# Performance work log

Hardware: AMD Instinct MI355X
Metric: run time of the kernel (lower is better)

The kernel has to match this reference:

```python
import jax, jax.numpy as jnp
import numpy as np

N_NODES = 50000
N_EDGES = 800000
F_IN = 128
HIDDEN = 128
F_OUT = 64
BN_EPS = 1e-5


def setup_inputs() -> dict:
    key = jax.random.key(0)
    ks = jax.random.split(key, 8)
    features = jax.random.normal(ks[0], (N_NODES, F_IN), dtype=jnp.float32)
    W1 = jax.random.normal(ks[1], (2 * F_IN, HIDDEN), dtype=jnp.float32) * 0.05
    b1 = jnp.zeros((HIDDEN,), dtype=jnp.float32)
    gamma = jnp.ones((HIDDEN,), dtype=jnp.float32)
    beta = jnp.zeros((HIDDEN,), dtype=jnp.float32)
    W2 = jax.random.normal(ks[2], (2 * HIDDEN, F_OUT), dtype=jnp.float32) * 0.05
    b2 = jnp.zeros((F_OUT,), dtype=jnp.float32)
    edge_vals = jax.random.uniform(ks[3], (N_EDGES,), dtype=jnp.float32)
    edge_src = jax.random.randint(ks[4], (N_EDGES,), 0, N_NODES, dtype=jnp.int32)
    edge_dst = jax.random.randint(ks[5], (N_EDGES,), 0, N_NODES, dtype=jnp.int32)
    return {"features": features, "W1": W1, "b1": b1, "gamma": gamma,
            "beta": beta, "W2": W2, "b2": b2, "edge_vals": edge_vals,
            "edge_src": edge_src, "edge_dst": edge_dst}


def _spmm(edge_vals, edge_src, edge_dst, x):
    # agg[i] = sum_{e: dst_e == i} w_e * x[src_e]   (sparse adjacency @ x)
    msgs = edge_vals[:, None] * x[edge_src]          # [E, d]
    return jax.ops.segment_sum(msgs, edge_dst, num_segments=N_NODES)


def _batchnorm(x, gamma, beta):
    # BatchNorm1d in training mode: batch stats, biased variance
    mean = jnp.mean(x, axis=0)
    var = jnp.mean(jnp.square(x - mean), axis=0)
    return gamma * (x - mean) * jax.lax.rsqrt(var + BN_EPS) + beta


def reference(features, W1, b1, gamma, beta, W2, b2, edge_vals, edge_src, edge_dst):
    # Layer 1: SpMM -> concat -> linear -> batchnorm -> relu  (dropout is a no-op, p=0)
    agg = _spmm(edge_vals, edge_src, edge_dst, features)     # [N, F_IN]
    s = jnp.concatenate([agg, features], axis=1)             # [N, 2*F_IN]
    h = s @ W1 + b1                                          # [N, HIDDEN]
    h = jax.nn.relu(_batchnorm(h, gamma, beta))
    # Layer 2: SpMM -> concat -> linear (identity act, no norm)
    agg2 = _spmm(edge_vals, edge_src, edge_dst, h)           # [N, HIDDEN]
    s2 = jnp.concatenate([agg2, h], axis=1)                  # [N, 2*HIDDEN]
    out = s2 @ W2 + b2                                       # [N, F_OUT]
    return out
```

## Files before the change

### kernel.cpp

```cpp
#include <hip/hip_runtime.h>

#define N_NODES 50000
#define N_EDGES 800000
#define F_IN    128
#define HID     128
#define F_OUT   64
#define BN_EPS  1e-5f

#define NRANGES 196
#define NCHUNKS 196
#define CHUNK   4096

typedef __bf16 bf16x8 __attribute__((ext_vector_type(8)));
typedef float  f32x4  __attribute__((ext_vector_type(4)));

static inline size_t align_up(size_t x, size_t a){ return (x + a - 1) / a * a; }

__device__ __forceinline__ float bflo(unsigned u){ return __uint_as_float(u << 16); }
__device__ __forceinline__ float bfhi(unsigned u){ return __uint_as_float(u & 0xffff0000u); }
__device__ __forceinline__ unsigned packbf(float a, float b){
  __bf16 ha = (__bf16)a, hb = (__bf16)b;
  unsigned short ua = __builtin_bit_cast(unsigned short, ha);
  unsigned short ub = __builtin_bit_cast(unsigned short, hb);
  return (unsigned)ua | ((unsigned)ub << 16);
}


__global__ __launch_bounds__(256) void k_pass1(const int* __restrict__ dst, int* __restrict__ Hcr){
  __shared__ int hist[NRANGES];
  int c = blockIdx.x, t = threadIdx.x;
  if(t < NRANGES) hist[t] = 0;
  __syncthreads();
  int e0 = c * CHUNK;
  #pragma unroll
  for(int k = 0; k < CHUNK / 256; k++){
    int e = e0 + k * 256 + t;
    if(e < N_EDGES) atomicAdd(&hist[dst[e] >> 8], 1);
  }
  __syncthreads();
  if(t < NRANGES) Hcr[c * NRANGES + t] = hist[t];
}

__global__ __launch_bounds__(256) void k_scanH(int* __restrict__ Hcr, int* __restrict__ rangeScan,
                                               float* __restrict__ bn_acc){
  __shared__ int s[256];
  int t = threadIdx.x;
  int run = 0;
  if(t < NRANGES){
    for(int c = 0; c < NCHUNKS; c++){
      int v = Hcr[c * NRANGES + t];
      Hcr[c * NRANGES + t] = run;
      run += v;
    }
  }
  s[t] = (t < NRANGES) ? run : 0;
  __syncthreads();
  for(int off = 1; off < 256; off <<= 1){
    int v = (t >= off) ? s[t - off] : 0;
    __syncthreads();
    s[t] += v;
    __syncthreads();
  }
  if(t < NRANGES) rangeScan[t + 1] = s[t];
  if(t == 0) rangeScan[0] = 0;
  bn_acc[t] = 0.f;
}

__global__ __launch_bounds__(256) void k_pass2(const int* __restrict__ dst, const int* __restrict__ src,
    const float* __restrict__ vals, const int* __restrict__ Hcr,
    const int* __restrict__ rangeScan, int2* __restrict__ staged){
  __shared__ int cur[NRANGES];
  int c = blockIdx.x, t = threadIdx.x;
  if(t < NRANGES) cur[t] = rangeScan[t] + Hcr[c * NRANGES + t];
  __syncthreads();
  int e0 = c * CHUNK;
  #pragma unroll
  for(int k = 0; k < CHUNK / 256; k++){
    int e = e0 + k * 256 + t;
    if(e < N_EDGES){
      int d = dst[e];
      int pos = atomicAdd(&cur[d >> 8], 1);
      staged[pos] = make_int2(__float_as_int(vals[e]), src[e] | ((d & 255) << 16));
    }
  }
}

__global__ __launch_bounds__(256) void k_pass3(const int2* __restrict__ staged,
    const int* __restrict__ rangeScan, int2* __restrict__ epack, int* __restrict__ rp){
  __shared__ int cnt[256];
  __shared__ int pre[256];
  int r = blockIdx.x, t = threadIdx.x;
  int beg = rangeScan[r], end = rangeScan[r + 1];
  cnt[t] = 0;
  __syncthreads();
  for(int i = beg + t; i < end; i += 256)
    atomicAdd(&cnt[(staged[i].y >> 16) & 255], 1);
  __syncthreads();
  int v = cnt[t];
  pre[t] = v;
  __syncthreads();
  for(int off = 1; off < 256; off <<= 1){
    int u = (t >= off) ? pre[t - off] : 0;
    __syncthreads();
    pre[t] += u;
    __syncthreads();
  }
  int excl = pre[t] - v;
  int d = r * 256 + t;
  if(d < N_NODES) rp[d] = beg + excl;
  if(r == NRANGES - 1 && t == 0) rp[N_NODES] = N_EDGES;
  __syncthreads();
  cnt[t] = beg + excl;
  __syncthreads();
  for(int i = beg + t; i < end; i += 256){
    int2 e = staged[i];
    int dl = (e.y >> 16) & 255;
    int p = atomicAdd(&cnt[dl], 1);
    epack[p] = make_int2(e.x, e.y & 0xffff);
  }
}


__global__ void k_prepW(const float* __restrict__ W1, const float* __restrict__ W2,
                        __bf16* __restrict__ W1f, __bf16* __restrict__ W2f){
  int t = blockIdx.x * 256 + threadIdx.x;
  if(t < 4096){
    int ks = t >> 9, rem = t & 511, nf = rem >> 6, l = rem & 63;
    int k = ks * 32 + (l >> 4) * 8, c = nf * 16 + (l & 15);
    bf16x8 v;
    #pragma unroll
    for(int i = 0; i < 8; i++) v[i] = (__bf16)W1[(size_t)(k + i) * HID + c];
    *(bf16x8*)(W1f + ((size_t)t << 3)) = v;
  } else if(t < 6144){
    int s = t - 4096;
    int ks = s >> 9, rem = s & 511, nf = rem >> 6, l = rem & 63;
    int k = ks * 32 + (l >> 4) * 8, c = nf * 16 + (l & 15);
    bf16x8 v;
    #pragma unroll
    for(int i = 0; i < 8; i++){
      int kk = k + i;
      float val = (c < 64) ? W2[(size_t)kk * F_OUT + c]
                           : W2[(size_t)(HID + kk) * F_OUT + (c - 64)];
      v[i] = (__bf16)val;
    }
    *(bf16x8*)(W2f + ((size_t)s << 3)) = v;
  }
}


__global__ __launch_bounds__(256) void k_cvtX(const float* __restrict__ X, __bf16* __restrict__ Sx){
  int t = blockIdx.x * 256 + threadIdx.x;
  if(t >= N_NODES * 16) return;
  int n = t >> 4;
  int c = (t & 15) * 8;
  const float* xp = X + (size_t)n * F_IN + c;
  f32x4 x0 = *(const f32x4*)xp;
  f32x4 x1 = *(const f32x4*)(xp + 4);
  bf16x8 v;
  #pragma unroll
  for(int i = 0; i < 4; i++){ v[i] = (__bf16)x0[i]; v[4 + i] = (__bf16)x1[i]; }
  *(bf16x8*)(Sx + (size_t)n * 128 + c) = v;
}


__global__ __launch_bounds__(256) void k_spmm1(const __bf16* __restrict__ Sx,
    __bf16* __restrict__ Sa, const int2* __restrict__ epack, const int* __restrict__ rp){
  int w    = (int)((blockIdx.x * blockDim.x + threadIdx.x) >> 6);
  int lane = threadIdx.x & 63;
  if(w >= N_NODES) return;
  int beg = rp[w], end = rp[w + 1];
  float a0 = 0.f, a1 = 0.f;
  int e = beg;
  for(; e + 3 < end; e += 4){
    int2 p0 = epack[e], p1 = epack[e + 1], p2 = epack[e + 2], p3 = epack[e + 3];
    unsigned u0 = *(const unsigned*)(Sx + (size_t)p0.y * 128 + lane * 2);
    unsigned u1 = *(const unsigned*)(Sx + (size_t)p1.y * 128 + lane * 2);
    unsigned u2 = *(const unsigned*)(Sx + (size_t)p2.y * 128 + lane * 2);
    unsigned u3 = *(const unsigned*)(Sx + (size_t)p3.y * 128 + lane * 2);
    float w0 = __int_as_float(p0.x), w1 = __int_as_float(p1.x);
    float w2 = __int_as_float(p2.x), w3 = __int_as_float(p3.x);
    a0 = fmaf(w0, bflo(u0), a0); a1 = fmaf(w0, bfhi(u0), a1);
    a0 = fmaf(w1, bflo(u1), a0); a1 = fmaf(w1, bfhi(u1), a1);
    a0 = fmaf(w2, bflo(u2), a0); a1 = fmaf(w2, bfhi(u2), a1);
    a0 = fmaf(w3, bflo(u3), a0); a1 = fmaf(w3, bfhi(u3), a1);
  }
  for(; e < end; e++){
    int2 p = epack[e];
    float wt = __int_as_float(p.x);
    unsigned u = *(const unsigned*)(Sx + (size_t)p.y * 128 + lane * 2);
    a0 = fmaf(wt, bflo(u), a0); a1 = fmaf(wt, bfhi(u), a1);
  }
  *(unsigned*)(Sa + (size_t)w * 128 + lane * 2) = packbf(a0, a1);
}


__global__ __launch_bounds__(256) void k_gemm1(
    const __bf16* __restrict__ Sa, const __bf16* __restrict__ Sx,
    const __bf16* __restrict__ W1f, const float* __restrict__ b1,
    __bf16* __restrict__ hpre, float* __restrict__ bn_acc){
  __shared__ float bnred[2][256];
  const int tid = threadIdx.x;
  const int lane = tid & 63, wid = tid >> 6;
  const int wm = wid >> 1, wn = wid & 1;
  const int lr = lane & 15, lk = (lane >> 4) * 8;
  const int rbase = blockIdx.x * 64 + wm * 32 + lr;

  f32x4 acc[2][4];
  #pragma unroll
  for(int m = 0; m < 2; m++)
    #pragma unroll
    for(int n = 0; n < 4; n++) acc[m][n] = (f32x4){0.f, 0.f, 0.f, 0.f};

  for(int ks = 0; ks < 8; ks++){
    const __bf16* src = (ks < 4) ? Sa : Sx;
    const int kb = (ks & 3) * 32 + lk;
    bf16x8 a[2], b[4];
    #pragma unroll
    for(int m = 0; m < 2; m++){
      int r = rbase + m * 16; if(r > N_NODES - 1) r = N_NODES - 1;
      a[m] = *(const bf16x8*)(src + (size_t)r * 128 + kb);
    }
    #pragma unroll
    for(int n = 0; n < 4; n++)
      b[n] = *(const bf16x8*)(W1f + (((ks * 8 + wn * 4 + n) * 64 + lane) << 3));
    #pragma unroll
    for(int m = 0; m < 2; m++)
      #pragma unroll
      for(int n = 0; n < 4; n++)
        acc[m][n] = __builtin_amdgcn_mfma_f32_16x16x32_bf16(a[m], b[n], acc[m][n], 0, 0, 0);
  }

  #pragma unroll
  for(int n = 0; n < 4; n++){
    int gc = wn * 64 + n * 16 + lr;
    float bias = b1[gc];
    float ps = 0.f, pq = 0.f;
    #pragma unroll
    for(int m = 0; m < 2; m++){
      int gr0 = blockIdx.x * 64 + wm * 32 + m * 16 + (lane >> 4) * 4;
      #pragma unroll
      for(int i = 0; i < 4; i++){
        int r = gr0 + i;
        if(r < N_NODES){
          float h = acc[m][n][i] + bias;
          hpre[(size_t)r * HID + gc] = (__bf16)h;
          ps += h; pq += h * h;
        }
      }
    }
    ps += __shfl_xor(ps, 16); ps += __shfl_xor(ps, 32);
    pq += __shfl_xor(pq, 16); pq += __shfl_xor(pq, 32);
    if(lane < 16){
      bnred[wm][gc] = ps;
      bnred[wm][128 + gc] = pq;
    }
  }
  __syncthreads();
  atomicAdd(&bn_acc[tid], bnred[0][tid] + bnred[1][tid]);
}


__global__ void k_bnstats(const float* __restrict__ bn_acc, const float* __restrict__ gamma,
                          const float* __restrict__ beta, float* __restrict__ bn_sc){
  int c = threadIdx.x;
  if(c < HID){
    float mean = bn_acc[c] / (float)N_NODES;
    float var  = bn_acc[HID + c] / (float)N_NODES - mean * mean;
    float rs   = rsqrtf(var + BN_EPS);
    float sc   = gamma[c] * rs;
    bn_sc[c]       = sc;
    bn_sc[HID + c] = beta[c] - mean * sc;
  }
}


__global__ __launch_bounds__(256) void k_gemm2(
    const __bf16* __restrict__ hpre, const __bf16* __restrict__ W2f,
    const float* __restrict__ b2, const float* __restrict__ bn_sc,
    __bf16* __restrict__ y2b, float* __restrict__ out){
  const int tid = threadIdx.x;
  const int lane = tid & 63, wid = tid >> 6;
  const int wm = wid >> 1, wn = wid & 1;
  const int lr = lane & 15, lk = (lane >> 4) * 8;
  const int rbase = blockIdx.x * 64 + wm * 32 + lr;

  f32x4 acc[2][4];
  #pragma unroll
  for(int m = 0; m < 2; m++)
    #pragma unroll
    for(int n = 0; n < 4; n++) acc[m][n] = (f32x4){0.f, 0.f, 0.f, 0.f};

  for(int ks = 0; ks < 4; ks++){
    int k0 = ks * 32 + lk;
    f32x4 sc0 = *(const f32x4*)(bn_sc + k0);
    f32x4 sc1 = *(const f32x4*)(bn_sc + k0 + 4);
    f32x4 sh0 = *(const f32x4*)(bn_sc + 128 + k0);
    f32x4 sh1 = *(const f32x4*)(bn_sc + 128 + k0 + 4);
    bf16x8 a[2], b[4];
    #pragma unroll
    for(int m = 0; m < 2; m++){
      int r = rbase + m * 16; if(r > N_NODES - 1) r = N_NODES - 1;
      bf16x8 hv = *(const bf16x8*)(hpre + (size_t)r * HID + k0);
      bf16x8 af;
      #pragma unroll
      for(int i = 0; i < 4; i++){
        af[i]     = (__bf16)fmaxf(0.f, fmaf((float)hv[i],     sc0[i], sh0[i]));
        af[4 + i] = (__bf16)fmaxf(0.f, fmaf((float)hv[4 + i], sc1[i], sh1[i]));
      }
      a[m] = af;
    }
    #pragma unroll
    for(int n = 0; n < 4; n++)
      b[n] = *(const bf16x8*)(W2f + (((ks * 8 + wn * 4 + n) * 64 + lane) << 3));
    #pragma unroll
    for(int m = 0; m < 2; m++)
      #pragma unroll
      for(int n = 0; n < 4; n++)
        acc[m][n] = __builtin_amdgcn_mfma_f32_16x16x32_bf16(a[m], b[n], acc[m][n], 0, 0, 0);
  }

  #pragma unroll
  for(int n = 0; n < 4; n++){
    int c = n * 16 + lr;
    float bias = (wn == 1) ? b2[c] : 0.f;
    #pragma unroll
    for(int m = 0; m < 2; m++){
      int gr0 = blockIdx.x * 64 + wm * 32 + m * 16 + (lane >> 4) * 4;
      #pragma unroll
      for(int i = 0; i < 4; i++){
        int r = gr0 + i;
        if(r < N_NODES){
          if(wn == 0) y2b[(size_t)r * F_OUT + c] = (__bf16)acc[m][n][i];
          else        out[(size_t)r * F_OUT + c] = acc[m][n][i] + bias;
        }
      }
    }
  }
}


__global__ __launch_bounds__(256) void k_spmm2(const __bf16* __restrict__ y2b,
    const int2* __restrict__ epack, const int* __restrict__ rp, float* __restrict__ out){
  int w    = (int)((blockIdx.x * blockDim.x + threadIdx.x) >> 6);
  int lane = threadIdx.x & 63;
  if(w >= N_NODES) return;
  int beg = rp[w], end = rp[w + 1];
  int half = lane >> 5, li = lane & 31;
  float a0 = 0.f, a1 = 0.f;
  int e = beg + half;
  for(; e + 2 < end; e += 4){
    int2 p0 = epack[e], p1 = epack[e + 2];
    float w0 = __int_as_float(p0.x), w1 = __int_as_float(p1.x);
    unsigned u0 = *(const unsigned*)(y2b + (size_t)p0.y * F_OUT + li * 2);
    unsigned u1 = *(const unsigned*)(y2b + (size_t)p1.y * F_OUT + li * 2);
    a0 = fmaf(w0, bflo(u0), a0); a1 = fmaf(w0, bfhi(u0), a1);
    a0 = fmaf(w1, bflo(u1), a0); a1 = fmaf(w1, bfhi(u1), a1);
  }
  if(e < end){
    int2 p = epack[e];
    float wt = __int_as_float(p.x);
    unsigned u = *(const unsigned*)(y2b + (size_t)p.y * F_OUT + li * 2);
    a0 = fmaf(wt, bflo(u), a0); a1 = fmaf(wt, bfhi(u), a1);
  }
  a0 += __shfl_xor(a0, 32);
  a1 += __shfl_xor(a1, 32);
  if(lane < 32){
    float2 o = *(float2*)(out + (size_t)w * F_OUT + li * 2);
    o.x += a0; o.y += a1;
    *(float2*)(out + (size_t)w * F_OUT + li * 2) = o;
  }
}


extern "C" void kernel_launch(void* const* d_in, const int* in_sizes, int n_in,
                              void* d_out, int out_size, void* d_ws, size_t ws_size,
                              hipStream_t stream){
  const float* X     = (const float*)d_in[0];
  const float* W1    = (const float*)d_in[1];
  const float* b1    = (const float*)d_in[2];
  const float* gamma = (const float*)d_in[3];
  const float* beta  = (const float*)d_in[4];
  const float* W2    = (const float*)d_in[5];
  const float* b2    = (const float*)d_in[6];
  const float* evals = (const float*)d_in[7];
  const int*   esrc  = (const int*)d_in[8];
  const int*   edst  = (const int*)d_in[9];
  float* out = (float*)d_out;

  char* ws = (char*)d_ws;
  size_t off = 0;
  auto carve = [&](size_t bytes) -> char* {
    off = align_up(off, 256);
    char* p = ws + off;
    off += bytes;
    return p;
  };
  int*     Hcr    = (int*)    carve((size_t)NCHUNKS * NRANGES * 4);
  int*     rscan  = (int*)    carve((size_t)(NRANGES + 1) * 4);
  int*     rp     = (int*)    carve(((size_t)N_NODES + 1) * 4);
  float*   bn_acc = (float*)  carve(256 * 4);
  float*   bn_sc  = (float*)  carve(256 * 4);
  int2*    staged = (int2*)   carve((size_t)N_EDGES * 8);
  int2*    epack  = (int2*)   carve((size_t)N_EDGES * 8);
  __bf16*  W1f    = (__bf16*) carve((size_t)4096 * 8 * 2);
  __bf16*  W2f    = (__bf16*) carve((size_t)2048 * 8 * 2);
  __bf16*  Sa     = (__bf16*) carve((size_t)N_NODES * 128 * 2);
  __bf16*  Sx     = (__bf16*) carve((size_t)N_NODES * 128 * 2);
  __bf16*  hpre   = (__bf16*) carve((size_t)N_NODES * HID * 2);
  __bf16*  y2b    = (__bf16*) carve((size_t)N_NODES * F_OUT * 2);

  k_pass1<<<NCHUNKS, 256, 0, stream>>>(edst, Hcr);
  k_scanH<<<1, 256, 0, stream>>>(Hcr, rscan, bn_acc);
  k_pass2<<<NCHUNKS, 256, 0, stream>>>(edst, esrc, evals, Hcr, rscan, staged);
  k_pass3<<<NRANGES, 256, 0, stream>>>(staged, rscan, epack, rp);

  k_prepW<<<24, 256, 0, stream>>>(W1, W2, W1f, W2f);
  k_cvtX<<<(N_NODES * 16 + 255) / 256, 256, 0, stream>>>(X, Sx);

  k_spmm1<<<N_NODES / 4, 256, 0, stream>>>(Sx, Sa, epack, rp);
  k_gemm1<<<(N_NODES + 63) / 64, 256, 0, stream>>>(Sa, Sx, W1f, b1, hpre, bn_acc);
  k_bnstats<<<1, 128, 0, stream>>>(bn_acc, gamma, beta, bn_sc);
  k_gemm2<<<(N_NODES + 63) / 64, 256, 0, stream>>>(hpre, W2f, b2, bn_sc, y2b, out);
  k_spmm2<<<N_NODES / 4, 256, 0, stream>>>(y2b, epack, rp, out);
}
```

Measured before the change: 255.7 us.

## Merge setup kernels, parallelize range scan, fold BN stats into gemm2

Folds the edge histogram, the X-to-bf16 conversion and the weight repacking into one launch with disjoint block roles. The single-block serial column scan is replaced by a per-range parallel scan across 196 blocks. The range prefix is now recomputed redundantly inside pass2 and pass3. The BN scale and shift computation moves into each gemm2 block's shared memory, so the separate stats kernel is gone. Together these remove three launches and a serial single-block bottleneck, at the cost of redundant per-block scans.

```diff
diff --git a/kernel.cpp b/kernel.cpp
--- a/kernel.cpp
+++ b/kernel.cpp
@@ -10,6 +10,8 @@
 #define NRANGES 196
 #define NCHUNKS 196
 #define CHUNK   4096
+#define CVT_BLOCKS 3125
+#define PREPW_BLOCKS 24
 
 typedef __bf16 bf16x8 __attribute__((ext_vector_type(8)));
 typedef float  f32x4  __attribute__((ext_vector_type(4)));
@@ -26,52 +28,97 @@
 }
 
 
-__global__ __launch_bounds__(256) void k_pass1(const int* __restrict__ dst, int* __restrict__ Hcr){
+__global__ __launch_bounds__(256) void k_setup(
+    const int* __restrict__ dst, const float* __restrict__ X,
+    const float* __restrict__ W1, const float* __restrict__ W2,
+    int* __restrict__ Hcr, __bf16* __restrict__ Sx,
+    __bf16* __restrict__ W1f, __bf16* __restrict__ W2f, float* __restrict__ bn_acc){
   __shared__ int hist[NRANGES];
-  int c = blockIdx.x, t = threadIdx.x;
-  if(t < NRANGES) hist[t] = 0;
-  __syncthreads();
-  int e0 = c * CHUNK;
-  #pragma unroll
-  for(int k = 0; k < CHUNK / 256; k++){
-    int e = e0 + k * 256 + t;
-    if(e < N_EDGES) atomicAdd(&hist[dst[e] >> 8], 1);
-  }
-  __syncthreads();
-  if(t < NRANGES) Hcr[c * NRANGES + t] = hist[t];
-}
-
-__global__ __launch_bounds__(256) void k_scanH(int* __restrict__ Hcr, int* __restrict__ rangeScan,
-                                               float* __restrict__ bn_acc){
+  int b = blockIdx.x, t = threadIdx.x;
+  if(b < NCHUNKS){
+    if(t < NRANGES) hist[t] = 0;
+    __syncthreads();
+    int e0 = b * CHUNK;
+    #pragma unroll
+    for(int k = 0; k < CHUNK / 256; k++){
+      int e = e0 + k * 256 + t;
+      if(e < N_EDGES) atomicAdd(&hist[dst[e] >> 8], 1);
+    }
+    __syncthreads();
+    if(t < NRANGES) Hcr[b * NRANGES + t] = hist[t];
+  } else if(b < NCHUNKS + CVT_BLOCKS){
+    int bb = b - NCHUNKS;
+    if(bb == 0) bn_acc[t] = 0.f;
+    int idx = bb * 256 + t;
+    int n = idx >> 4;
+    int c = (idx & 15) * 8;
+    const float* xp = X + (size_t)n * F_IN + c;
+    f32x4 x0 = *(const f32x4*)xp;
+    f32x4 x1 = *(const f32x4*)(xp + 4);
+    bf16x8 v;
+    #pragma unroll
+    for(int i = 0; i < 4; i++){ v[i] = (__bf16)x0[i]; v[4 + i] = (__bf16)x1[i]; }
+    *(bf16x8*)(Sx + (size_t)n * 128 + c) = v;
+  } else {
+    int s = (b - NCHUNKS - CVT_BLOCKS) * 256 + t;
+    if(s < 4096){
+      int ks = s >> 9, rem = s & 511, nf = rem >> 6, l = rem & 63;
+      int k = ks * 32 + (l >> 4) * 8, c = nf * 16 + (l & 15);
+      bf16x8 v;
+      #pragma unroll
+      for(int i = 0; i < 8; i++) v[i] = (__bf16)W1[(size_t)(k + i) * HID + c];
+      *(bf16x8*)(W1f + ((size_t)s << 3)) = v;
+    } else {
+      int q = s - 4096;
+      int ks = q >> 9, rem = q & 511, nf = rem >> 6, l = rem & 63;
+      int k = ks * 32 + (l >> 4) * 8, c = nf * 16 + (l & 15);
+      bf16x8 v;
+      #pragma unroll
+      for(int i = 0; i < 8; i++){
+        int kk = k + i;
+        float val = (c < 64) ? W2[(size_t)kk * F_OUT + c]
+                             : W2[(size_t)(HID + kk) * F_OUT + (c - 64)];
+        v[i] = (__bf16)val;
+      }
+      *(bf16x8*)(W2f + ((size_t)q << 3)) = v;
+    }
+  }
+}
+
+
+__global__ __launch_bounds__(256) void k_scanR(int* __restrict__ Hcr, int* __restrict__ rtot){
   __shared__ int s[256];
-  int t = threadIdx.x;
-  int run = 0;
-  if(t < NRANGES){
-    for(int c = 0; c < NCHUNKS; c++){
-      int v = Hcr[c * NRANGES + t];
-      Hcr[c * NRANGES + t] = run;
-      run += v;
-    }
-  }
-  s[t] = (t < NRANGES) ? run : 0;
+  int r = blockIdx.x, t = threadIdx.x;
+  int v = (t < NCHUNKS) ? Hcr[t * NRANGES + r] : 0;
+  s[t] = v;
   __syncthreads();
   for(int off = 1; off < 256; off <<= 1){
-    int v = (t >= off) ? s[t - off] : 0;
-    __syncthreads();
-    s[t] += v;
-    __syncthreads();
-  }
-  if(t < NRANGES) rangeScan[t + 1] = s[t];
-  if(t == 0) rangeScan[0] = 0;
-  bn_acc[t] = 0.f;
-}
+    int u = (t >= off) ? s[t - off] : 0;
+    __syncthreads();
+    s[t] += u;
+    __syncthreads();
+  }
+  if(t < NCHUNKS) Hcr[t * NRANGES + r] = s[t] - v;
+  if(t == NCHUNKS - 1) rtot[r] = s[t];
+}
+
 
 __global__ __launch_bounds__(256) void k_pass2(const int* __restrict__ dst, const int* __restrict__ src,
     const float* __restrict__ vals, const int* __restrict__ Hcr,
-    const int* __restrict__ rangeScan, int2* __restrict__ staged){
+    const int* __restrict__ rtot, int2* __restrict__ staged){
+  __shared__ int s[256];
   __shared__ int cur[NRANGES];
   int c = blockIdx.x, t = threadIdx.x;
-  if(t < NRANGES) cur[t] = rangeScan[t] + Hcr[c * NRANGES + t];
+  int tv = (t < NRANGES) ? rtot[t] : 0;
+  s[t] = tv;
+  __syncthreads();
+  for(int off = 1; off < 256; off <<= 1){
+    int u = (t >= off) ? s[t - off] : 0;
+    __syncthreads();
+    s[t] += u;
+    __syncthreads();
+  }
+  if(t < NRANGES) cur[t] = (s[t] - tv) + Hcr[c * NRANGES + t];
   __syncthreads();
   int e0 = c * CHUNK;
   #pragma unroll
@@ -85,27 +132,39 @@
   }
 }
 
+
 __global__ __launch_bounds__(256) void k_pass3(const int2* __restrict__ staged,
-    const int* __restrict__ rangeScan, int2* __restrict__ epack, int* __restrict__ rp){
+    const int* __restrict__ rtot, int2* __restrict__ epack, int* __restrict__ rp){
+  __shared__ int s[256];
   __shared__ int cnt[256];
-  __shared__ int pre[256];
+  __shared__ int begS, endS;
   int r = blockIdx.x, t = threadIdx.x;
-  int beg = rangeScan[r], end = rangeScan[r + 1];
+  int tv = (t < NRANGES) ? rtot[t] : 0;
+  s[t] = tv;
+  __syncthreads();
+  for(int off = 1; off < 256; off <<= 1){
+    int u = (t >= off) ? s[t - off] : 0;
+    __syncthreads();
+    s[t] += u;
+    __syncthreads();
+  }
+  if(t == r){ begS = s[t] - tv; endS = s[t]; }
   cnt[t] = 0;
   __syncthreads();
+  int beg = begS, end = endS;
   for(int i = beg + t; i < end; i += 256)
     atomicAdd(&cnt[(staged[i].y >> 16) & 255], 1);
   __syncthreads();
   int v = cnt[t];
-  pre[t] = v;
+  s[t] = v;
   __syncthreads();
   for(int off = 1; off < 256; off <<= 1){
-    int u = (t >= off) ? pre[t - off] : 0;
-    __syncthreads();
-    pre[t] += u;
-    __syncthreads();
-  }
-  int excl = pre[t] - v;
+    int u = (t >= off) ? s[t - off] : 0;
+    __syncthreads();
+    s[t] += u;
+    __syncthreads();
+  }
+  int excl = s[t] - v;
   int d = r * 256 + t;
   if(d < N_NODES) rp[d] = beg + excl;
   if(r == NRANGES - 1 && t == 0) rp[N_NODES] = N_EDGES;
@@ -118,48 +177,6 @@
     int p = atomicAdd(&cnt[dl], 1);
     epack[p] = make_int2(e.x, e.y & 0xffff);
   }
-}
-
-
-__global__ void k_prepW(const float* __restrict__ W1, const float* __restrict__ W2,
-                        __bf16* __restrict__ W1f, __bf16* __restrict__ W2f){
-  int t = blockIdx.x * 256 + threadIdx.x;
-  if(t < 4096){
-    int ks = t >> 9, rem = t & 511, nf = rem >> 6, l = rem & 63;
-    int k = ks * 32 + (l >> 4) * 8, c = nf * 16 + (l & 15);
-    bf16x8 v;
-    #pragma unroll
-    for(int i = 0; i < 8; i++) v[i] = (__bf16)W1[(size_t)(k + i) * HID + c];
-    *(bf16x8*)(W1f + ((size_t)t << 3)) = v;
-  } else if(t < 6144){
-    int s = t - 4096;
-    int ks = s >> 9, rem = s & 511, nf = rem >> 6, l = rem & 63;
-    int k = ks * 32 + (l >> 4) * 8, c = nf * 16 + (l & 15);
-    bf16x8 v;
-    #pragma unroll
-    for(int i = 0; i < 8; i++){
-      int kk = k + i;
-      float val = (c < 64) ? W2[(size_t)kk * F_OUT + c]
-                           : W2[(size_t)(HID + kk) * F_OUT + (c - 64)];
-      v[i] = (__bf16)val;
-    }
-    *(bf16x8*)(W2f + ((size_t)s << 3)) = v;
-  }
-}
-
-
-__global__ __launch_bounds__(256) void k_cvtX(const float* __restrict__ X, __bf16* __restrict__ Sx){
-  int t = blockIdx.x * 256 + threadIdx.x;
-  if(t >= N_NODES * 16) return;
-  int n = t >> 4;
-  int c = (t & 15) * 8;
-  const float* xp = X + (size_t)n * F_IN + c;
-  f32x4 x0 = *(const f32x4*)xp;
-  f32x4 x1 = *(const f32x4*)(xp + 4);
-  bf16x8 v;
-  #pragma unroll
-  for(int i = 0; i < 4; i++){ v[i] = (__bf16)x0[i]; v[4 + i] = (__bf16)x1[i]; }
-  *(bf16x8*)(Sx + (size_t)n * 128 + c) = v;
 }
 
 
@@ -260,25 +277,21 @@
 }
 
 
-__global__ void k_bnstats(const float* __restrict__ bn_acc, const float* __restrict__ gamma,
-                          const float* __restrict__ beta, float* __restrict__ bn_sc){
-  int c = threadIdx.x;
-  if(c < HID){
-    float mean = bn_acc[c] / (float)N_NODES;
-    float var  = bn_acc[HID + c] / (float)N_NODES - mean * mean;
-    float rs   = rsqrtf(var + BN_EPS);
-    float sc   = gamma[c] * rs;
-    bn_sc[c]       = sc;
-    bn_sc[HID + c] = beta[c] - mean * sc;
-  }
-}
-
-
 __global__ __launch_bounds__(256) void k_gemm2(
     const __bf16* __restrict__ hpre, const __bf16* __restrict__ W2f,
-    const float* __restrict__ b2, const float* __restrict__ bn_sc,
+    const float* __restrict__ b2, const float* __restrict__ bn_acc,
+    const float* __restrict__ gamma, const float* __restrict__ beta,
     __bf16* __restrict__ y2b, float* __restrict__ out){
+  __shared__ float s_scale[HID], s_shift[HID];
   const int tid = threadIdx.x;
+  if(tid < HID){
+    float mean = bn_acc[tid] / (float)N_NODES;
+    float var  = bn_acc[HID + tid] / (float)N_NODES - mean * mean;
+    float rs   = rsqrtf(var + BN_EPS);
+    float sc   = gamma[tid] * rs;
+    s_scale[tid] = sc;
+    s_shift[tid] = beta[tid] - mean * sc;
+  }
   const int lane = tid & 63, wid = tid >> 6;
   const int wm = wid >> 1, wn = wid & 1;
   const int lr = lane & 15, lk = (lane >> 4) * 8;
@@ -289,13 +302,14 @@
   for(int m = 0; m < 2; m++)
     #pragma unroll
     for(int n = 0; n < 4; n++) acc[m][n] = (f32x4){0.f, 0.f, 0.f, 0.f};
+  __syncthreads();
 
   for(int ks = 0; ks < 4; ks++){
     int k0 = ks * 32 + lk;
-    f32x4 sc0 = *(const f32x4*)(bn_sc + k0);
-    f32x4 sc1 = *(const f32x4*)(bn_sc + k0 + 4);
-    f32x4 sh0 = *(const f32x4*)(bn_sc + 128 + k0);
-    f32x4 sh1 = *(const f32x4*)(bn_sc + 128 + k0 + 4);
+    f32x4 sc0 = *(const f32x4*)(s_scale + k0);
+    f32x4 sc1 = *(const f32x4*)(s_scale + k0 + 4);
+    f32x4 sh0 = *(const f32x4*)(s_shift + k0);
+    f32x4 sh1 = *(const f32x4*)(s_shift + k0 + 4);
     bf16x8 a[2], b[4];
     #pragma unroll
     for(int m = 0; m < 2; m++){
@@ -396,10 +410,9 @@
     return p;
   };
   int*     Hcr    = (int*)    carve((size_t)NCHUNKS * NRANGES * 4);
-  int*     rscan  = (int*)    carve((size_t)(NRANGES + 1) * 4);
+  int*     rtot   = (int*)    carve((size_t)NRANGES * 4);
   int*     rp     = (int*)    carve(((size_t)N_NODES + 1) * 4);
   float*   bn_acc = (float*)  carve(256 * 4);
-  float*   bn_sc  = (float*)  carve(256 * 4);
   int2*    staged = (int2*)   carve((size_t)N_EDGES * 8);
   int2*    epack  = (int2*)   carve((size_t)N_EDGES * 8);
   __bf16*  W1f    = (__bf16*) carve((size_t)4096 * 8 * 2);
@@ -409,17 +422,14 @@
   __bf16*  hpre   = (__bf16*) carve((size_t)N_NODES * HID * 2);
   __bf16*  y2b    = (__bf16*) carve((size_t)N_NODES * F_OUT * 2);
 
-  k_pass1<<<NCHUNKS, 256, 0, stream>>>(edst, Hcr);
-  k_scanH<<<1, 256, 0, stream>>>(Hcr, rscan, bn_acc);
-  k_pass2<<<NCHUNKS, 256, 0, stream>>>(edst, esrc, evals, Hcr, rscan, staged);
-  k_pass3<<<NRANGES, 256, 0, stream>>>(staged, rscan, epack, rp);
-
-  k_prepW<<<24, 256, 0, stream>>>(W1, W2, W1f, W2f);
-  k_cvtX<<<(N_NODES * 16 + 255) / 256, 256, 0, stream>>>(X, Sx);
+  k_setup<<<NCHUNKS + CVT_BLOCKS + PREPW_BLOCKS, 256, 0, stream>>>(
+      edst, X, W1, W2, Hcr, Sx, W1f, W2f, bn_acc);
+  k_scanR<<<NRANGES, 256, 0, stream>>>(Hcr, rtot);
+  k_pass2<<<NCHUNKS, 256, 0, stream>>>(edst, esrc, evals, Hcr, rtot, staged);
+  k_pass3<<<NRANGES, 256, 0, stream>>>(staged, rtot, epack, rp);
 
   k_spmm1<<<N_NODES / 4, 256, 0, stream>>>(Sx, Sa, epack, rp);
   k_gemm1<<<(N_NODES + 63) / 64, 256, 0, stream>>>(Sa, Sx, W1f, b1, hpre, bn_acc);
-  k_bnstats<<<1, 128, 0, stream>>>(bn_acc, gamma, beta, bn_sc);
-  k_gemm2<<<(N_NODES + 63) / 64, 256, 0, stream>>>(hpre, W2f, b2, bn_sc, y2b, out);
+  k_gemm2<<<(N_NODES + 63) / 64, 256, 0, stream>>>(hpre, W2f, b2, bn_acc, gamma, beta, y2b, out);
   k_spmm2<<<N_NODES / 4, 256, 0, stream>>>(y2b, epack, rp, out);
 }
```

New measurement: 245.7 us. 3.9% less time.
